# Optimization experiments

Measured on AMD Instinct MI355X. Metric: run time of the kernel, lower is better.

Reference implementation:

```python
import jax, jax.numpy as jnp
import numpy as np

LEAKAGE = 0.9
RADIUS = 0.1
AVG_DEGREE = 6


def setup_inputs() -> dict:
    key = jax.random.key(0)
    k1, k2, k3, k4, k5 = jax.random.split(key, 5)
    B, T, I, N, O = 16, 2048, 32, 2048, 32
    input_sequence = jax.random.normal(k1, (B, T, I), dtype=jnp.float32)
    # sparse reservoir matrix, uniform(-1,1) with density avg_degree/N, scaled to spectral radius
    A = jax.random.uniform(k2, (N, N), minval=-1.0, maxval=1.0, dtype=jnp.float32)
    mask = jax.random.uniform(k3, (N, N)) < (AVG_DEGREE / N)
    A = jnp.where(mask, A, 0.0)
    # approximate spectral normalization (power-iteration-free surrogate scale)
    A = A * (RADIUS / jnp.max(jnp.abs(jnp.linalg.eigvals(A))).astype(jnp.float32))
    Win = (RADIUS) * (2.0 * jax.random.uniform(k4, (N, I), dtype=jnp.float32) - 1.0)
    Wout_w = jax.random.normal(k5, (O, N), dtype=jnp.float32) / np.sqrt(N)
    return {"input_sequence": input_sequence, "Win": Win, "A": A, "Wout_w": Wout_w, "washout_len": 64}


def reference(input_sequence, Win, A, Wout_w, washout_len):
    # input projection for all timesteps at once (noise_std = 0.0)
    inp = jnp.einsum('bti,ni->btn', input_sequence, Win)  # [B, T, N]
    B = input_sequence.shape[0]
    N = A.shape[0]
    h0 = jnp.zeros((B, N), dtype=input_sequence.dtype)
    At = A.T

    def step(h, u_t):
        # h: [B, N], u_t: [B, N]
        h_new = (1.0 - LEAKAGE) * h + LEAKAGE * jnp.tanh(h @ At + u_t)
        return h_new, h_new

    _, hs = jax.lax.scan(step, h0, jnp.swapaxes(inp, 0, 1))  # hs: [T, B, N]
    hs = jnp.swapaxes(hs, 0, 1)  # [B, T, N]
    h_list = hs[:, washout_len - 1:]  # keep steps i >= washout_len - 1
    return jnp.einsum('btn,on->bto', h_list, Wout_w)
```

## Files before the change

### kernel.cpp

```cpp
#include <hip/hip_runtime.h>
#include <stdint.h>

#define BB 16
#define TT 2048
#define NI 32
#define NN 2048
#define NO 32
#define WASH 64
#define TO (TT - WASH + 1)
#define W 24
#define WT 24
#define CH 16
#define HBST 2056
#define HBROW 4112
#define UROWB 4132
#define U2OFF 65792
#define LDS_BYTES (U2OFF + CH*UROWB)

typedef short bfvec __attribute__((ext_vector_type(8)));
typedef float f4_t  __attribute__((ext_vector_type(4)));

__device__ inline unsigned short f2bf(float f) {
  unsigned int u = __builtin_bit_cast(unsigned int, f);
  unsigned int r = u + 0x7fffu + ((u >> 16) & 1u);
  return (unsigned short)(r >> 16);
}
__device__ inline float bf2f(unsigned short s) {
  unsigned int u = ((unsigned int)s) << 16;
  return __builtin_bit_cast(float, u);
}
__device__ inline float tanh_fast(float x) {
  x = fminf(15.f, fmaxf(-15.f, x));
  float e = __expf(x + x);
  float r = __builtin_amdgcn_rcpf(e + 1.0f);
  return (e - 1.0f) * r;
}

__global__ void build_ell(const float* __restrict__ A, uint32_t* __restrict__ ell,
                          uint32_t* __restrict__ deg) {
  int gw = (int)((blockIdx.x * blockDim.x + threadIdx.x) >> 6);
  int lane = (int)(threadIdx.x & 63);
  if (gw >= NN) return;
  const float* row = A + (size_t)gw * NN;
  int base = 0;
  for (int c = 0; c < NN; c += 64) {
    float v = row[c + lane];
    bool nz = (v != 0.0f);
    unsigned long long mask = __ballot(nz);
    int pre = __popcll(mask & ((1ull << lane) - 1ull));
    if (nz) {
      int idx = base + pre;
      if (idx < W) {
        uint32_t packed = (((uint32_t)f2bf(v)) << 16) | (uint32_t)((c + lane) * 4);
        ell[(size_t)gw * W + idx] = packed;
      }
    }
    base += __popcll(mask);
  }
  int d = base < W ? base : W;
  if (lane == 0) deg[gw] = (uint32_t)d;
  for (int k = d + lane; k < W; k += 64) ell[(size_t)gw * W + k] = 0u;
}

__global__ void sortperm(const uint32_t* __restrict__ deg, uint32_t* __restrict__ perm,
                         uint32_t* __restrict__ invp) {
  __shared__ int dg[NN];
  int tid = (int)threadIdx.x;
  dg[tid] = (int)deg[tid];
  dg[tid + 1024] = (int)deg[tid + 1024];
  __syncthreads();
  for (int r = tid; r < NN; r += 1024) {
    int d = dg[r];
    int rank = 0;
    for (int j = 0; j < NN; ++j) {
      int dj = dg[j];
      rank += (dj < d) || (dj == d && j < r);
    }
    perm[rank] = (uint32_t)r;
    invp[r] = (uint32_t)rank;
  }
}

__global__ void pairsort(const uint32_t* __restrict__ deg, const uint32_t* __restrict__ perm,
                         uint32_t* __restrict__ pairrank, uint32_t* __restrict__ pp) {
  __shared__ int ps[1024];
  int p = (int)threadIdx.x;
  int d0 = (int)deg[perm[p]]; if (d0 > W) d0 = W;
  int d1 = (int)deg[perm[2047 - p]]; if (d1 > W) d1 = W;
  int s = d0 + d1; if (s > WT) s = WT;
  ps[p] = s;
  __syncthreads();
  int rank = 0;
  for (int j = 0; j < 1024; ++j) {
    int sj = ps[j];
    rank += (sj < s) || (sj == s && j < p);
  }
  pairrank[p] = (uint32_t)rank;
  pp[rank] = (uint32_t)p;
}

__device__ inline int rank2pos(int r, const uint32_t* pairrank) {
  return (r < 1024) ? (2 * (int)pairrank[r]) : (2 * (int)pairrank[2047 - r] + 1);
}

__global__ void build_pairs(const uint32_t* __restrict__ ell, const uint32_t* __restrict__ deg,
                            const uint32_t* __restrict__ perm, const uint32_t* __restrict__ invp,
                            const uint32_t* __restrict__ pairrank, const uint32_t* __restrict__ pp,
                            uint32_t* __restrict__ pa, uint32_t* __restrict__ pva,
                            uint32_t* __restrict__ pvb, uint32_t* __restrict__ wavecnt) {
  int blk = (int)blockIdx.x;
  int lane = (int)threadIdx.x;
  int t = blk * 64 + lane;
  int p = (int)pp[t];
  uint32_t a_[WT], u_[WT], w_[WT];
  int n = 0;
  int ro = (int)perm[p];
  int d = (int)deg[ro]; if (d > W) d = W;
  for (int k = 0; k < d && n < WT; ++k) {
    uint32_t e = ell[(size_t)ro * W + k];
    int pos = rank2pos((int)invp[(e & 0xffffu) >> 2], pairrank);
    a_[n] = (uint32_t)(pos * 2);
    u_[n] = e & 0xffff0000u;
    w_[n] = 0u;
    ++n;
  }
  ro = (int)perm[2047 - p];
  d = (int)deg[ro]; if (d > W) d = W;
  for (int k = 0; k < d && n < WT; ++k) {
    uint32_t e = ell[(size_t)ro * W + k];
    int pos = rank2pos((int)invp[(e & 0xffffu) >> 2], pairrank);
    a_[n] = (uint32_t)(pos * 2);
    u_[n] = 0u;
    w_[n] = e & 0xffff0000u;
    ++n;
  }
  int cnt = n;
  for (int i = 1; i < cnt; ++i) {
    uint32_t aa = a_[i], uu = u_[i], ww = w_[i];
    uint32_t key = (((aa >> 2) & 31u) - (uint32_t)lane) & 31u;
    int j = i - 1;
    while (j >= 0 && ((((a_[j] >> 2) & 31u) - (uint32_t)lane) & 31u) > key) {
      a_[j + 1] = a_[j]; u_[j + 1] = u_[j]; w_[j + 1] = w_[j]; --j;
    }
    a_[j + 1] = aa; u_[j + 1] = uu; w_[j + 1] = ww;
  }
  for (n = cnt; n < WT; ++n) {
    a_[n] = (uint32_t)(((lane + n) & 31) << 2);
    u_[n] = 0u; w_[n] = 0u;
  }
  int m = cnt;
  #pragma unroll
  for (int off = 32; off; off >>= 1) m = max(m, __shfl_xor(m, off));
  if (lane == 0) wavecnt[blk] = (uint32_t)m;
  for (int k = 0; k < WT; ++k) {
    pa[(size_t)t * WT + k] = a_[k];
    pva[(size_t)t * WT + k] = u_[k];
    pvb[(size_t)t * WT + k] = w_[k];
  }
}

__global__ void build_frags(const float* __restrict__ Win, const float* __restrict__ Wout,
                            const uint32_t* __restrict__ perm, const uint32_t* __restrict__ pp,
                            uint32_t* __restrict__ winf, uint32_t* __restrict__ woutf) {
  int f = (int)(blockIdx.x * blockDim.x + threadIdx.x);
  if (f < 32768) {
    int reg = f & 3, lane = (f >> 2) & 63, ntg = f >> 8;
    int n = (ntg << 4) + (lane & 15);
    int k = ((lane >> 4) << 3) + reg * 2;
    int p = (int)pp[n >> 1];
    int np = (int)perm[(n & 1) ? (2047 - p) : p];
    uint32_t lo = f2bf(Win[(size_t)np * NI + k]);
    uint32_t hi = f2bf(Win[(size_t)np * NI + k + 1]);
    winf[f] = lo | (hi << 16);
  } else {
    int g = f - 32768;
    int reg = g & 3, lane = (g >> 2) & 63, kt = (g >> 8) & 63, ot = g >> 14;
    int o = (ot << 4) + (lane & 15);
    int n = (kt << 5) + ((lane >> 4) << 3) + reg * 2;
    int p = (int)pp[n >> 1];
    int n0 = (int)perm[p];
    int n1 = (int)perm[2047 - p];
    uint32_t lo = f2bf(Wout[(size_t)o * NN + n0]);
    uint32_t hi = f2bf(Wout[(size_t)o * NN + n1]);
    woutf[g] = lo | (hi << 16);
  }
}

#define ENT(K, BASE)                                                                 \
  {                                                                                  \
    float hv = bf2f(*(const unsigned short*)(smem + (BASE) + ea##K));                \
    y0 = __builtin_fmaf(__builtin_bit_cast(float, va##K), hv, y0);                   \
    y1 = __builtin_fmaf(__builtin_bit_cast(float, vb##K), hv, y1);                   \
  }

#define ENTS8(B)  ENT(0,B) ENT(1,B) ENT(2,B) ENT(3,B) ENT(4,B) ENT(5,B) ENT(6,B) ENT(7,B)
#define ENTS10(B) ENTS8(B)  ENT(8,B)  ENT(9,B)
#define ENTS12(B) ENTS10(B) ENT(10,B) ENT(11,B)
#define ENTS14(B) ENTS12(B) ENT(12,B) ENT(13,B)
#define ENTS16(B) ENTS14(B) ENT(14,B) ENT(15,B)
#define ENTS18(B) ENTS16(B) ENT(16,B) ENT(17,B)
#define ENTS20(B) ENTS18(B) ENT(18,B) ENT(19,B)
#define ENTS22(B) ENTS20(B) ENT(20,B) ENT(21,B)
#define ENTS24(B) ENTS22(B) ENT(22,B) ENT(23,B)

#define STEPLOOP(ENTS)                                                               \
  _Pragma("unroll 1")                                                                \
  for (int tt = 0; tt < CH; ++tt) {                                                  \
    const int po = ((tt + CH - 1) & (CH - 1)) * HBROW;                               \
    uint32_t uw = *(const uint32_t*)(smem + u2a + tt * UROWB);                       \
    float y0 = bf2f((unsigned short)(uw & 0xffffu));                                 \
    float y1 = bf2f((unsigned short)(uw >> 16));                                     \
    ENTS(po)                                                                         \
    float hn0 = 0.1f * h0 + 0.9f * tanh_fast(y0);                                    \
    float hn1 = 0.1f * h1 + 0.9f * tanh_fast(y1);                                    \
    *(uint32_t*)(smem + hwa + tt * HBROW) =                                          \
        (uint32_t)f2bf(hn0) | ((uint32_t)f2bf(hn1) << 16);                           \
    h0 = hn0; h1 = hn1;                                                              \
    __syncthreads();                                                                 \
  }

__global__ __launch_bounds__(1024, 1) void rec_kernel(
    const float* __restrict__ x,
    const uint32_t* __restrict__ pa, const uint32_t* __restrict__ pva,
    const uint32_t* __restrict__ pvb, const uint32_t* __restrict__ wavecnt,
    const uint32_t* __restrict__ winf, const uint32_t* __restrict__ woutf,
    float* __restrict__ out) {
  extern __shared__ char smem[];
  unsigned short* hb = (unsigned short*)smem;
  float* oscratch = (float*)(smem + U2OFF);

  const int tid = (int)threadIdx.x;
  const int b = (int)blockIdx.x;
  const int lane = tid & 63;
  const int wv = tid >> 6;
  const int la15 = lane & 15;
  const int lg = lane >> 4;
  const int u2a = U2OFF + (tid << 2);
  const int hwa = tid << 2;

  int cnt = __builtin_amdgcn_readfirstlane((int)wavecnt[wv]);

  uint32_t ea0, ea1, ea2, ea3, ea4, ea5, ea6, ea7, ea8, ea9, ea10, ea11,
           ea12, ea13, ea14, ea15, ea16, ea17, ea18, ea19, ea20, ea21, ea22, ea23;
  uint32_t va0, va1, va2, va3, va4, va5, va6, va7, va8, va9, va10, va11,
           va12, va13, va14, va15, va16, va17, va18, va19, va20, va21, va22, va23;
  uint32_t vb0, vb1, vb2, vb3, vb4, vb5, vb6, vb7, vb8, vb9, vb10, vb11,
           vb12, vb13, vb14, vb15, vb16, vb17, vb18, vb19, vb20, vb21, vb22, vb23;
  {
    const uint4* qa = (const uint4*)(pa + (size_t)tid * WT);
    const uint4* qv = (const uint4*)(pva + (size_t)tid * WT);
    const uint4* qw = (const uint4*)(pvb + (size_t)tid * WT);
    uint4 A0 = qa[0], A1 = qa[1], A2 = qa[2], A3 = qa[3], A4 = qa[4], A5 = qa[5];
    uint4 V0 = qv[0], V1 = qv[1], V2 = qv[2], V3 = qv[3], V4 = qv[4], V5 = qv[5];
    uint4 B0 = qw[0], B1 = qw[1], B2 = qw[2], B3 = qw[3], B4 = qw[4], B5 = qw[5];
    ea0 = A0.x; ea1 = A0.y; ea2 = A0.z; ea3 = A0.w;
    ea4 = A1.x; ea5 = A1.y; ea6 = A1.z; ea7 = A1.w;
    ea8 = A2.x; ea9 = A2.y; ea10 = A2.z; ea11 = A2.w;
    ea12 = A3.x; ea13 = A3.y; ea14 = A3.z; ea15 = A3.w;
    ea16 = A4.x; ea17 = A4.y; ea18 = A4.z; ea19 = A4.w;
    ea20 = A5.x; ea21 = A5.y; ea22 = A5.z; ea23 = A5.w;
    va0 = V0.x; va1 = V0.y; va2 = V0.z; va3 = V0.w;
    va4 = V1.x; va5 = V1.y; va6 = V1.z; va7 = V1.w;
    va8 = V2.x; va9 = V2.y; va10 = V2.z; va11 = V2.w;
    va12 = V3.x; va13 = V3.y; va14 = V3.z; va15 = V3.w;
    va16 = V4.x; va17 = V4.y; va18 = V4.z; va19 = V4.w;
    va20 = V5.x; va21 = V5.y; va22 = V5.z; va23 = V5.w;
    vb0 = B0.x; vb1 = B0.y; vb2 = B0.z; vb3 = B0.w;
    vb4 = B1.x; vb5 = B1.y; vb6 = B1.z; vb7 = B1.w;
    vb8 = B2.x; vb9 = B2.y; vb10 = B2.z; vb11 = B2.w;
    vb12 = B3.x; vb13 = B3.y; vb14 = B3.z; vb15 = B3.w;
    vb16 = B4.x; vb17 = B4.y; vb18 = B4.z; vb19 = B4.w;
    vb20 = B5.x; vb21 = B5.y; vb22 = B5.z; vb23 = B5.w;
  }

  *(uint32_t*)(smem + (CH - 1) * HBROW + (tid << 2)) = 0u;
  float h0 = 0.0f, h1 = 0.0f;

  for (int c = 0; c < TT / CH; ++c) {
    const int t0 = c * CH;

    {
      const float* xp = x + ((size_t)b * TT + (t0 + la15)) * NI + (lg << 3);
      float4 x0 = *(const float4*)xp;
      float4 x1 = *(const float4*)(xp + 4);
      union { unsigned short u16[8]; bfvec v; } af;
      af.u16[0]=f2bf(x0.x); af.u16[1]=f2bf(x0.y); af.u16[2]=f2bf(x0.z); af.u16[3]=f2bf(x0.w);
      af.u16[4]=f2bf(x1.x); af.u16[5]=f2bf(x1.y); af.u16[6]=f2bf(x1.z); af.u16[7]=f2bf(x1.w);
      #pragma unroll
      for (int nt = 0; nt < 8; ++nt) {
        int ntg = (wv << 3) + nt;
        union { uint4 q; bfvec v; } bw;
        bw.q = *(const uint4*)(winf + (((size_t)ntg * 64 + lane) << 2));
        f4_t acc = {0.f, 0.f, 0.f, 0.f};
        acc = __builtin_amdgcn_mfma_f32_16x16x32_bf16(bw.v, af.v, acc, 0, 0, 0);
        int dw = (ntg << 3) + (lg << 1);
        uint32_t w0 = (uint32_t)f2bf(acc[0]) | ((uint32_t)f2bf(acc[1]) << 16);
        uint32_t w1 = (uint32_t)f2bf(acc[2]) | ((uint32_t)f2bf(acc[3]) << 16);
        char* ub = smem + U2OFF + la15 * UROWB + (dw << 2);
        *(uint32_t*)(ub) = w0;
        *(uint32_t*)(ub + 4) = w1;
      }
    }
    __syncthreads();

    asm volatile("" : "+s"(cnt));
    if      (cnt <= 8)  { STEPLOOP(ENTS8)  }
    else if (cnt <= 10) { STEPLOOP(ENTS10) }
    else if (cnt <= 12) { STEPLOOP(ENTS12) }
    else if (cnt <= 14) { STEPLOOP(ENTS14) }
    else if (cnt <= 16) { STEPLOOP(ENTS16) }
    else if (cnt <= 18) { STEPLOOP(ENTS18) }
    else if (cnt <= 20) { STEPLOOP(ENTS20) }
    else if (cnt <= 22) { STEPLOOP(ENTS22) }
    else                { STEPLOOP(ENTS24) }

    {
      f4_t oa0 = {0.f,0.f,0.f,0.f}, oa1 = {0.f,0.f,0.f,0.f};
      #pragma unroll
      for (int k4 = 0; k4 < 4; ++k4) {
        int kt = (wv << 2) + k4;
        union { uint4 q; bfvec v; } ha, w0, w1;
        ha.q = *(const uint4*)(hb + (size_t)la15 * HBST + (kt << 5) + (lg << 3));
        w0.q = *(const uint4*)(woutf + (((size_t)(kt) * 64 + lane) << 2));
        w1.q = *(const uint4*)(woutf + (((size_t)(64 + kt) * 64 + lane) << 2));
        oa0 = __builtin_amdgcn_mfma_f32_16x16x32_bf16(ha.v, w0.v, oa0, 0, 0, 0);
        oa1 = __builtin_amdgcn_mfma_f32_16x16x32_bf16(ha.v, w1.v, oa1, 0, 0, 0);
      }
      float* os = oscratch + (wv << 9);
      int tb = lg << 2;
      #pragma unroll
      for (int r = 0; r < 4; ++r) os[(tb + r) * 32 + la15] = oa0[r];
      #pragma unroll
      for (int r = 0; r < 4; ++r) os[(tb + r) * 32 + 16 + la15] = oa1[r];
    }
    __syncthreads();
    if (tid < 512) {
      float s = 0.0f;
      #pragma unroll
      for (int w2 = 0; w2 < 16; ++w2) s += oscratch[(w2 << 9) + tid];
      int tg = t0 + (tid >> 5);
      if (tg >= WASH - 1)
        out[((size_t)b * TO + (tg - (WASH - 1))) * NO + (tid & 31)] = s;
    }
    __syncthreads();
  }
}

extern "C" void kernel_launch(void* const* d_in, const int* in_sizes, int n_in,
                              void* d_out, int out_size, void* d_ws, size_t ws_size,
                              hipStream_t stream) {
  (void)in_sizes; (void)n_in; (void)out_size; (void)ws_size;
  const float* x    = (const float*)d_in[0];
  const float* Win  = (const float*)d_in[1];
  const float* A    = (const float*)d_in[2];
  const float* Wout = (const float*)d_in[3];
  float* out = (float*)d_out;

  char* ws = (char*)d_ws;
  uint32_t* ell      = (uint32_t*)(ws);
  uint32_t* deg      = (uint32_t*)(ws + 196608);
  uint32_t* perm     = (uint32_t*)(ws + 204800);
  uint32_t* invp     = (uint32_t*)(ws + 212992);
  uint32_t* pairrank = (uint32_t*)(ws + 221184);
  uint32_t* pp       = (uint32_t*)(ws + 225280);
  uint32_t* wavecnt  = (uint32_t*)(ws + 229376);
  uint32_t* pa       = (uint32_t*)(ws + 229504);
  uint32_t* pva      = (uint32_t*)(ws + 327808);
  uint32_t* pvb      = (uint32_t*)(ws + 426112);
  uint32_t* winf     = (uint32_t*)(ws + 524416);
  uint32_t* woutf    = (uint32_t*)(ws + 655488);

  hipFuncSetAttribute((const void*)rec_kernel,
                      hipFuncAttributeMaxDynamicSharedMemorySize, 160 * 1024);

  hipLaunchKernelGGL(build_ell, dim3(512), dim3(256), 0, stream, A, ell, deg);
  hipLaunchKernelGGL(sortperm, dim3(1), dim3(1024), 0, stream, deg, perm, invp);
  hipLaunchKernelGGL(pairsort, dim3(1), dim3(1024), 0, stream, deg, perm, pairrank, pp);
  hipLaunchKernelGGL(build_pairs, dim3(16), dim3(64), 0, stream,
                     ell, deg, perm, invp, pairrank, pp, pa, pva, pvb, wavecnt);
  hipLaunchKernelGGL(build_frags, dim3(256), dim3(256), 0, stream, Win, Wout, perm, pp, winf, woutf);
  hipLaunchKernelGGL(rec_kernel, dim3(16), dim3(1024), LDS_BYTES, stream,
                     x, pa, pva, pvb, wavecnt, winf, woutf, out);
}
```

Measured before the change: 2.919 ms.

## Schedule per-wave gather slots to balance LDS banks and round slot counts

Replaces the per-lane rotation sort of neighbor entries with a wave-cooperative greedy scheduler. It assigns each slot's gather so that each of 32 LDS banks gets at most two lanes per step, using ballots to count bank usage. It also rounds the per-wave slot count up to an even value. The aim is to cut LDS bank conflicts in the main recurrent SpMV loop. The setup kernel becomes more expensive, and forced placements can still conflict.

```diff
diff --git a/kernel.cpp b/kernel.cpp
--- a/kernel.cpp
+++ b/kernel.cpp
@@ -103,6 +103,10 @@
   return (r < 1024) ? (2 * (int)pairrank[r]) : (2 * (int)pairrank[2047 - r] + 1);
 }
 
+__device__ inline int bcnt_get(unsigned long long lo, unsigned long long hi, int b) {
+  return (int)(((b < 16) ? (lo >> (4 * b)) : (hi >> (4 * (b - 16)))) & 15ull);
+}
+
 __global__ void build_pairs(const uint32_t* __restrict__ ell, const uint32_t* __restrict__ deg,
                             const uint32_t* __restrict__ perm, const uint32_t* __restrict__ invp,
                             const uint32_t* __restrict__ pairrank, const uint32_t* __restrict__ pp,
@@ -113,49 +117,93 @@
   int t = blk * 64 + lane;
   int p = (int)pp[t];
   uint32_t a_[WT], u_[WT], w_[WT];
-  int n = 0;
-  int ro = (int)perm[p];
-  int d = (int)deg[ro]; if (d > W) d = W;
-  for (int k = 0; k < d && n < WT; ++k) {
-    uint32_t e = ell[(size_t)ro * W + k];
-    int pos = rank2pos((int)invp[(e & 0xffffu) >> 2], pairrank);
-    a_[n] = (uint32_t)(pos * 2);
-    u_[n] = e & 0xffff0000u;
-    w_[n] = 0u;
-    ++n;
-  }
-  ro = (int)perm[2047 - p];
-  d = (int)deg[ro]; if (d > W) d = W;
-  for (int k = 0; k < d && n < WT; ++k) {
-    uint32_t e = ell[(size_t)ro * W + k];
-    int pos = rank2pos((int)invp[(e & 0xffffu) >> 2], pairrank);
-    a_[n] = (uint32_t)(pos * 2);
-    u_[n] = 0u;
-    w_[n] = e & 0xffff0000u;
-    ++n;
-  }
-  int cnt = n;
-  for (int i = 1; i < cnt; ++i) {
-    uint32_t aa = a_[i], uu = u_[i], ww = w_[i];
-    uint32_t key = (((aa >> 2) & 31u) - (uint32_t)lane) & 31u;
-    int j = i - 1;
-    while (j >= 0 && ((((a_[j] >> 2) & 31u) - (uint32_t)lane) & 31u) > key) {
-      a_[j + 1] = a_[j]; u_[j + 1] = u_[j]; w_[j + 1] = w_[j]; --j;
-    }
-    a_[j + 1] = aa; u_[j + 1] = uu; w_[j + 1] = ww;
-  }
-  for (n = cnt; n < WT; ++n) {
-    a_[n] = (uint32_t)(((lane + n) & 31) << 2);
-    u_[n] = 0u; w_[n] = 0u;
+  int cnt = 0;
+  {
+    int ro = (int)perm[p];
+    int d = (int)deg[ro]; if (d > W) d = W;
+    for (int k = 0; k < d && cnt < WT; ++k) {
+      uint32_t e = ell[(size_t)ro * W + k];
+      int pos = rank2pos((int)invp[(e & 0xffffu) >> 2], pairrank);
+      a_[cnt] = (uint32_t)(pos * 2);
+      u_[cnt] = e & 0xffff0000u;
+      w_[cnt] = 0u;
+      ++cnt;
+    }
+    ro = (int)perm[2047 - p];
+    d = (int)deg[ro]; if (d > W) d = W;
+    for (int k = 0; k < d && cnt < WT; ++k) {
+      uint32_t e = ell[(size_t)ro * W + k];
+      int pos = rank2pos((int)invp[(e & 0xffffu) >> 2], pairrank);
+      a_[cnt] = (uint32_t)(pos * 2);
+      u_[cnt] = 0u;
+      w_[cnt] = e & 0xffff0000u;
+      ++cnt;
+    }
   }
   int m = cnt;
   #pragma unroll
   for (int off = 32; off; off >>= 1) m = max(m, __shfl_xor(m, off));
-  if (lane == 0) wavecnt[blk] = (uint32_t)m;
+  int S = (m <= 8) ? 8 : (m <= 10) ? 10 : (m <= 12) ? 12 : (m <= 14) ? 14 :
+          (m <= 16) ? 16 : (m <= 18) ? 18 : (m <= 20) ? 20 : (m <= 22) ? 22 : 24;
+  if (lane == 0) wavecnt[blk] = (uint32_t)S;
+
+  uint32_t sa[WT], su[WT], sw[WT];
+  for (int s = 0; s < WT; ++s) {
+    sa[s] = ((uint32_t)((lane + s) & 31)) << 2;
+    su[s] = 0u; sw[s] = 0u;
+  }
+  uint32_t used = 0;
+  for (int s = 0; s < S; ++s) {
+    unsigned long long clo = 0ull, chi = 0ull;
+    bool placed = false;
+    for (int round = 0; round < 3; ++round) {
+      int best = -1, bestc = 999;
+      if (!placed) {
+        for (int k = 0; k < WT; ++k) {
+          if (k >= cnt) break;
+          if ((used >> k) & 1u) continue;
+          int b = (int)((a_[k] >> 2) & 31u);
+          int c = bcnt_get(clo, chi, b);
+          if (c < bestc) { bestc = c; best = k; }
+        }
+      }
+      int pb = (best >= 0 && !placed) ? (int)((a_[best] >> 2) & 31u) : 32;
+      bool force = (round == 2);
+      for (int b = 0; b < 32; ++b) {
+        unsigned long long mb = __ballot(pb == b);
+        if (!mb) continue;
+        int have = bcnt_get(clo, chi, b);
+        int cap = 2 - have; if (cap < 0) cap = 0;
+        if (pb == b && !placed) {
+          int rank = __popcll(mb & ((1ull << (unsigned)lane) - 1ull));
+          if (force || rank < cap) {
+            placed = true;
+            used |= (1u << (unsigned)best);
+            sa[s] = a_[best]; su[s] = u_[best]; sw[s] = w_[best];
+          }
+        }
+        int nprop = (int)__popcll(mb);
+        int add = force ? nprop : (nprop < cap ? nprop : cap);
+        int room = 15 - have; if (add > room) add = room;
+        if (add > 0) {
+          if (b < 16) clo += ((unsigned long long)add) << (4 * b);
+          else        chi += ((unsigned long long)add) << (4 * (b - 16));
+        }
+      }
+    }
+    if (!placed) {
+      int pick = lane & 31;
+      for (int j = 0; j < 32; ++j) {
+        int b = (lane + j) & 31;
+        if (bcnt_get(clo, chi, b) < 2) { pick = b; break; }
+      }
+      sa[s] = ((uint32_t)pick) << 2;
+    }
+  }
   for (int k = 0; k < WT; ++k) {
-    pa[(size_t)t * WT + k] = a_[k];
-    pva[(size_t)t * WT + k] = u_[k];
-    pvb[(size_t)t * WT + k] = w_[k];
+    pa[(size_t)t * WT + k] = sa[k];
+    pva[(size_t)t * WT + k] = su[k];
+    pvb[(size_t)t * WT + k] = sw[k];
   }
 }
 
```

After: 2.798 ms. 4.1% less time.
